# Optimization experiments

Hardware: AMD Instinct MI355X
Metric: run time of the kernel (lower is better)

## Reference

```python
import math
import jax, jax.numpy as jnp
import numpy as np

B, DIM, C, N = 1024, 512, 1000, 8
R = 0.05
WEIGHT_LAMBDA = 0.3
CN = C * N
TOPK = math.ceil(R * CN)  # 400


def setup_inputs() -> dict:
    key = jax.random.key(0)
    k1, k2, k3 = jax.random.split(key, 3)
    x = jax.random.normal(k1, (B, DIM), dtype=jnp.float32)
    # kaiming_uniform_(a=sqrt(5)) on a (DIM, CN) tensor: fan_in = CN (torch 2D fan_in = size(1)),
    # gain = sqrt(2/(1+a^2)) = sqrt(1/3), bound = gain * sqrt(3/fan_in)
    bound = math.sqrt(1.0 / 3.0) * math.sqrt(3.0 / CN)
    proxies = jax.random.uniform(k2, (DIM, CN), dtype=jnp.float32, minval=-bound, maxval=bound)
    target = jax.random.randint(k3, (B,), 0, C)
    return {"x": x, "proxies": proxies, "target": target}


def reference(x, proxies, target):
    instance_label = jnp.repeat(jnp.arange(C), N)  # (CN,)

    # F.normalize(Proxies, p=2, dim=0) with eps=1e-12 clamp
    norm = jnp.maximum(jnp.linalg.norm(proxies, axis=0, keepdims=True), 1e-12)
    centers = proxies / norm  # (DIM, CN)

    similarity = x @ centers  # (B, CN)

    positive_mask = (target[:, None] == instance_label[None, :]).astype(similarity.dtype)

    # topk over similarity boosted so all positives are included, then scatter 1s
    _, idx = jax.lax.top_k(similarity + 1000.0 * positive_mask, TOPK)  # (B, TOPK)
    mask = jnp.zeros_like(similarity).at[jnp.arange(B)[:, None], idx].set(1.0)
    mask = jax.lax.stop_gradient(mask)

    prob_a = mask * similarity  # (B, CN)
    # matmul with block one-hot y_instance_onehot == sum over the N proxies of each class
    logits = prob_a.reshape(B, C, N).sum(axis=-1)  # (B, C)

    logits_mask = jax.lax.stop_gradient((logits != 0.0).astype(logits.dtype))
    exp_l = jnp.exp(logits) * logits_mask
    predict = exp_l / (1e-8 + exp_l.sum(axis=1, keepdims=True))

    # sum(-y_onehot * log(predict+1e-20), 1) == -log(predict[b, target[b]] + 1e-20)
    loss_classify = jnp.mean(-jnp.log(predict[jnp.arange(B), target] + 1e-20))

    # regularizer: (centers.T @ centers) @ y_instance_onehot, fused as
    # centers.T @ (per-class sum of centers) -- identical math, avoids the CNxCN matrix
    centers_cls = centers.reshape(DIM, C, N).sum(axis=-1)  # (DIM, C)
    centers_logits = centers.T @ centers_cls  # (CN, C)
    logp = jax.nn.log_softmax(centers_logits, axis=1)
    reg = -jnp.mean(logp[jnp.arange(CN), instance_label])

    total = loss_classify + WEIGHT_LAMBDA * reg
    return (total, loss_classify)
```

## Files before the change

### kernel.cpp

```cpp
#include <hip/hip_runtime.h>
#include <hip/hip_bf16.h>
#include <math.h>

#define PB   1024
#define PDIM 512
#define PC   1000
#define PN   8
#define PCN  8000
#define PTOPK 400
#define NONPOS_K 392
#define NBIN 1024
#define CANDMAX 1024

typedef __bf16 bf16x8 __attribute__((ext_vector_type(8)));
typedef __bf16 bf16x4 __attribute__((ext_vector_type(4)));
typedef float  f32x4  __attribute__((ext_vector_type(4)));

__device__ static inline void async_load16(const __bf16* g, __bf16* l) {
    __builtin_amdgcn_global_load_lds(
        (const __attribute__((address_space(1))) void*)g,
        (__attribute__((address_space(3))) void*)l,
        16, 0, 0);
}

__global__ __launch_bounds__(256) void k_pre(const float* __restrict__ x,
                                             const float* __restrict__ P,
                                             __bf16* __restrict__ xb,
                                             float* __restrict__ ssqp,
                                             float* __restrict__ esd,
                                             float* __restrict__ padf,
                                             float* __restrict__ acc) {
    int b = blockIdx.x, tid = threadIdx.x;
    if (b == 0 && tid < 8) acc[tid] = 0.f;
    if (b < 512) {
        int i = b * 256 + tid;
        float4 v = ((const float4*)x)[i];
        bf16x4 o;
        o[0] = (__bf16)v.x; o[1] = (__bf16)v.y; o[2] = (__bf16)v.z; o[3] = (__bf16)v.w;
        ((bf16x4*)xb)[i] = o;
    } else if (b < 768) {
        int idx = b - 512;
        int slice = idx & 7, jb = idx >> 3;
        int j = jb * 256 + tid;
        if (j < PCN) {
            const float* p = P + (size_t)(slice * 64) * PCN + j;
            float ss = 0.f;
#pragma unroll 8
            for (int r = 0; r < 64; ++r) {
                float v = p[(size_t)r * PCN];
                ss = fmaf(v, v, ss);
            }
            ssqp[slice * PCN + j] = ss;
        }
    } else {
        int i = (b - 768) * 256 + tid;
        if (i < 16000) esd[i] = 0.f;
        else if (i < 16000 + 6144) padf[i - 16000] = 0.f;
    }
}

__global__ __launch_bounds__(256) void k_tpose(const float* __restrict__ P,
                                               const float* __restrict__ ssqp,
                                               __bf16* __restrict__ Pt,
                                               __bf16* __restrict__ ccls) {
    __shared__ float t[64][65];
    __shared__ float sinv[64];
    int tid = threadIdx.x;
    int tx = tid & 63, ty = tid >> 6;
    int j0 = blockIdx.x * 64, d0 = blockIdx.y * 64;
    if (tid < 64) {
        float sq = 0.f;
#pragma unroll
        for (int p2 = 0; p2 < 8; ++p2) sq += ssqp[p2 * PCN + j0 + tid];
        sinv[tid] = 1.0f / fmaxf(sqrtf(sq), 1e-12f);
    }
#pragma unroll
    for (int r = 0; r < 16; ++r) {
        int d = d0 + ty * 16 + r;
        t[ty * 16 + r][tx] = P[(size_t)d * PCN + j0 + tx];
    }
    __syncthreads();
    float cs0 = 0.f, cs1 = 0.f;
#pragma unroll
    for (int r = 0; r < 16; ++r) {
        int jl = ty * 16 + r;
        float val = t[tx][jl] * sinv[jl];
        Pt[(size_t)(j0 + jl) * PDIM + d0 + tx] = (__bf16)val;
        if (r < 8) cs0 += val; else cs1 += val;
    }
    int c0 = (j0 >> 3) + ty * 2;
    ccls[(size_t)c0 * PDIM + d0 + tx] = (__bf16)cs0;
    ccls[(size_t)(c0 + 1) * PDIM + d0 + tx] = (__bf16)cs1;
}

__global__ __launch_bounds__(256, 2) void k_gemms(const __bf16* __restrict__ xb,
                                                  const __bf16* __restrict__ Pt,
                                                  const __bf16* __restrict__ ccls,
                                                  __bf16* __restrict__ simb,
                                                  float* __restrict__ esum,
                                                  float* __restrict__ diag) {
    __shared__ __bf16 Xs[2][128 * 32];
    __shared__ __bf16 Ps[2][128 * 32];
    __shared__ __bf16 Cs[2][128 * 32];
    int tid = threadIdx.x;
    int w = tid >> 6, lane = tid & 63;
    int wr = w >> 1, wc = w & 1;
    int quad = lane >> 4, l15 = lane & 15;
    int id = blockIdx.x;
    int jt = id >> 3, t = id & 7;
    int m0 = t * 128;
    int n0 = jt * 128;

    f32x4 accS[4][4] = {};
    f32x4 accC[4][4] = {};

#define STAGE3(buf, k0) {                                                     \
    _Pragma("unroll")                                                         \
    for (int pass = 0; pass < 2; ++pass) {                                    \
        int cc_ = pass * 256 + w * 64 + lane;                                 \
        int row_ = cc_ >> 2, ko_ = (cc_ & 3) * 8;                             \
        async_load16(xb + (size_t)(m0 + row_) * PDIM + (k0) + ko_,            \
                     &Xs[buf][cc_ * 8]);                                      \
        int prow = n0 + row_; if (prow > PCN - 1) prow = PCN - 1;             \
        async_load16(Pt + (size_t)prow * PDIM + (k0) + ko_,                   \
                     &Ps[buf][cc_ * 8]);                                      \
        async_load16(ccls + (size_t)(m0 + row_) * PDIM + (k0) + ko_,          \
                     &Cs[buf][cc_ * 8]);                                      \
    } }

    STAGE3(0, 0)
    for (int it = 0; it < 16; ++it) {
        int cur = it & 1;
        __syncthreads();
        if (it < 15) STAGE3(cur ^ 1, (it + 1) * 32)
        bf16x8 xa[4], pb[4], pa[4], cb[4];
#pragma unroll
        for (int i = 0; i < 4; ++i) {
            xa[i] = *(const bf16x8*)&Xs[cur][(wr * 64 + i * 16 + l15) * 32 + quad * 8];
            pb[i] = *(const bf16x8*)&Ps[cur][(wc * 64 + i * 16 + l15) * 32 + quad * 8];
            pa[i] = *(const bf16x8*)&Ps[cur][(wr * 64 + i * 16 + l15) * 32 + quad * 8];
            cb[i] = *(const bf16x8*)&Cs[cur][(wc * 64 + i * 16 + l15) * 32 + quad * 8];
        }
#pragma unroll
        for (int i = 0; i < 4; ++i)
#pragma unroll
            for (int j = 0; j < 4; ++j) {
                accS[i][j] = __builtin_amdgcn_mfma_f32_16x16x32_bf16(
                    xa[i], pb[j], accS[i][j], 0, 0, 0);
                accC[i][j] = __builtin_amdgcn_mfma_f32_16x16x32_bf16(
                    pa[i], cb[j], accC[i][j], 0, 0, 0);
            }
    }
#undef STAGE3

#pragma unroll
    for (int i = 0; i < 4; ++i) {
        int r0 = m0 + wr * 64 + i * 16 + quad * 4;
#pragma unroll
        for (int j = 0; j < 4; ++j) {
            int cc = n0 + wc * 64 + j * 16 + l15;
            if (cc < PCN) {
#pragma unroll
                for (int r = 0; r < 4; ++r)
                    simb[(size_t)(r0 + r) * PCN + cc] = (__bf16)accS[i][j][r];
            }
        }
    }
#pragma unroll
    for (int i = 0; i < 4; ++i) {
        int r0 = n0 + wr * 64 + i * 16 + quad * 4;
        float psum[4] = {0.f, 0.f, 0.f, 0.f};
#pragma unroll
        for (int j = 0; j < 4; ++j) {
            int cc = m0 + wc * 64 + j * 16 + l15;
            bool cvalid = (cc < PC);
#pragma unroll
            for (int r = 0; r < 4; ++r) {
                float v = accC[i][j][r];
                psum[r] += cvalid ? expf(v) : 0.f;
                int rr = r0 + r;
                if (cvalid && rr < PCN && cc == (rr >> 3)) diag[rr] = v;
            }
        }
#pragma unroll
        for (int off = 1; off < 16; off <<= 1)
#pragma unroll
            for (int r = 0; r < 4; ++r)
                psum[r] += __shfl_xor(psum[r], off, 64);
        if (l15 == 0) {
#pragma unroll
            for (int r = 0; r < 4; ++r) {
                int rr = r0 + r;
                if (rr < PCN) atomicAdd(&esum[rr], psum[r]);
            }
        }
    }
}

__global__ __launch_bounds__(256) void k_rowloss(const __bf16* __restrict__ sim,
                                                 const int* __restrict__ target,
                                                 float* __restrict__ acc) {
    __shared__ unsigned hist[NBIN];
    __shared__ float redf[8];
    __shared__ unsigned wtot[4];
    __shared__ float cand[CANDMAX];
    __shared__ unsigned candn;
    __shared__ int s_bin, s_A;
    __shared__ float s_tau;
    __shared__ int s_gt, s_eq;
    __shared__ float s_et;

    int b = blockIdx.x, tid = threadIdx.x;
    int lane = tid & 63, wv = tid >> 6;
    const bf16x8* row8 = (const bf16x8*)(sim + (size_t)b * PCN);
    int targ = target[b];

#pragma unroll
    for (int k = 0; k < 4; ++k) hist[tid + 256 * k] = 0u;
    if (tid == 0) candn = 0u;

    float pv[4][8];
    float lmn = INFINITY, lmx = -INFINITY;
#pragma unroll
    for (int k = 0; k < 4; ++k) {
        int c = tid + 256 * k;
        if (c < PC) {
            bf16x8 vv = row8[c];
#pragma unroll
            for (int n = 0; n < 8; ++n) pv[k][n] = (float)vv[n];
            if (c != targ) {
#pragma unroll
                for (int n = 0; n < 8; ++n) {
                    lmn = fminf(lmn, pv[k][n]);
                    lmx = fmaxf(lmx, pv[k][n]);
                }
            }
        } else {
#pragma unroll
            for (int n = 0; n < 8; ++n) pv[k][n] = 0.f;
        }
    }
    for (int off = 32; off; off >>= 1) {
        lmn = fminf(lmn, __shfl_down(lmn, off, 64));
        lmx = fmaxf(lmx, __shfl_down(lmx, off, 64));
    }
    if (lane == 0) { redf[wv] = lmn; redf[4 + wv] = lmx; }
    __syncthreads();
    float lo = fminf(fminf(redf[0], redf[1]), fminf(redf[2], redf[3]));
    float hi = fmaxf(fmaxf(redf[4], redf[5]), fmaxf(redf[6], redf[7]));
    float range = hi - lo;
    float scale = (range > 0.f) ? (float)NBIN / range : 0.f;

#pragma unroll
    for (int k = 0; k < 4; ++k) {
        int c = tid + 256 * k;
        if (c < PC && c != targ) {
#pragma unroll
            for (int n = 0; n < 8; ++n) {
                int bin = (int)((pv[k][n] - lo) * scale);
                bin = bin < 0 ? 0 : (bin > NBIN - 1 ? NBIN - 1 : bin);
                atomicAdd(&hist[bin], 1u);
            }
        }
    }
    __syncthreads();

    int b0 = tid * 4;
    unsigned h0 = hist[b0], h1 = hist[b0 + 1], h2 = hist[b0 + 2], h3 = hist[b0 + 3];
    unsigned l3 = h3, l2 = h2 + l3, l1 = h1 + l2, l0 = h0 + l1;
    unsigned T = l0;
#pragma unroll
    for (int step = 1; step < 64; step <<= 1) {
        unsigned u = __shfl_down(T, step, 64);
        if (lane + step < 64) T += u;
    }
    if (lane == 0) wtot[wv] = T;
    __syncthreads();
    unsigned tail = 0;
#pragma unroll
    for (int w2 = 0; w2 < 4; ++w2) if (w2 > wv) tail += wtot[w2];
    unsigned E = T - l0 + tail;
    {
        unsigned sfx[4] = {l0 + E, l1 + E, l2 + E, l3 + E};
        unsigned nxt[4] = {l1 + E, l2 + E, l3 + E, E};
#pragma unroll
        for (int i = 0; i < 4; ++i)
            if (sfx[i] >= NONPOS_K && nxt[i] < NONPOS_K) {
                s_bin = b0 + i;
                s_A = (int)nxt[i];
            }
    }
    __syncthreads();
    int tbin = s_bin, A = s_A;

#pragma unroll
    for (int k = 0; k < 4; ++k) {
        int c = tid + 256 * k;
        if (c < PC && c != targ) {
#pragma unroll
            for (int n = 0; n < 8; ++n) {
                int bin = (int)((pv[k][n] - lo) * scale);
                bin = bin < 0 ? 0 : (bin > NBIN - 1 ? NBIN - 1 : bin);
                if (bin == tbin) {
                    unsigned idx = atomicAdd(&candn, 1u);
                    if (idx < CANDMAX) cand[idx] = pv[k][n];
                }
            }
        }
    }
    __syncthreads();
    int m = (int)candn; if (m > CANDMAX) m = CANDMAX;
    int rank = NONPOS_K - A;
    for (int ci = tid; ci < m; ci += 256) {
        float val = cand[ci];
        int g = 0, e = 0;
        for (int i = 0; i < m; ++i) {
            g += cand[i] > val;
            e += cand[i] == val;
        }
        if (g < rank && rank <= g + e) { s_tau = val; s_gt = g; s_eq = e; }
    }
    __syncthreads();
    float tau = s_tau;
    int cgt = A + s_gt, ceq = s_eq;
    int rem = NONPOS_K - cgt;
    bool all_eq = (rem >= ceq);

    int offs[4] = {0, 0, 0, 0};
    if (!all_eq) {
        unsigned chunk_base = 0;
#pragma unroll
        for (int k = 0; k < 4; ++k) {
            int c = tid + 256 * k;
            unsigned tn = 0;
            if (c < PC && c != targ) {
#pragma unroll
                for (int n = 0; n < 8; ++n) tn += (pv[k][n] == tau) ? 1u : 0u;
            }
            unsigned inc = tn;
#pragma unroll
            for (int step = 1; step < 64; step <<= 1) {
                unsigned u = __shfl_up(inc, step, 64);
                if (lane >= step) inc += u;
            }
            __syncthreads();
            if (lane == 63) wtot[wv] = inc;
            __syncthreads();
            unsigned base = 0;
#pragma unroll
            for (int w2 = 0; w2 < 4; ++w2) if (w2 < wv) base += wtot[w2];
            offs[k] = (int)(chunk_base + base + inc - tn);
            chunk_base += wtot[0] + wtot[1] + wtot[2] + wtot[3];
        }
    }

    float psum = 0.f;
#pragma unroll
    for (int k = 0; k < 4; ++k) {
        int c = tid + 256 * k;
        if (c >= PC) continue;
        float lg = 0.f;
        if (c == targ) {
#pragma unroll
            for (int n = 0; n < 8; ++n) lg += pv[k][n];
        } else {
#pragma unroll
            for (int n = 0; n < 8; ++n) {
                float v = pv[k][n];
                bool sel = v > tau;
                if (!sel && v == tau) {
                    if (all_eq) sel = true;
                    else { sel = (offs[k] < rem); offs[k]++; }
                }
                if (sel) lg += v;
            }
        }
        float e = (lg != 0.0f) ? expf(lg) : 0.0f;
        psum += e;
        if (c == targ) s_et = e;
    }
    for (int off = 32; off; off >>= 1) psum += __shfl_down(psum, off, 64);
    if (lane == 0) redf[wv] = psum;
    __syncthreads();
    if (tid == 0) {
        float denom = 1e-8f + redf[0] + redf[1] + redf[2] + redf[3];
        atomicAdd(acc, -logf(s_et / denom + 1e-20f));
    }
}

__global__ __launch_bounds__(256) void k_final(const float* __restrict__ esum,
                                               const float* __restrict__ diag,
                                               const float* __restrict__ acc,
                                               float* __restrict__ out) {
    __shared__ float redf[4];
    int tid = threadIdx.x, lane = tid & 63, wv = tid >> 6;
    float s = 0.f;
    for (int j = tid; j < PCN; j += 256)
        s += logf(esum[j]) - diag[j];
    for (int off = 32; off; off >>= 1) s += __shfl_down(s, off, 64);
    if (lane == 0) redf[wv] = s;
    __syncthreads();
    if (tid == 0) {
        float rg = (redf[0] + redf[1] + redf[2] + redf[3]) * (1.0f / PCN);
        float lc = acc[0] * (1.0f / PB);
        out[0] = lc + 0.3f * rg;
        out[1] = lc;
    }
}

extern "C" void kernel_launch(void* const* d_in, const int* in_sizes, int n_in,
                              void* d_out, int out_size, void* d_ws, size_t ws_size,
                              hipStream_t stream) {
    const float* x       = (const float*)d_in[0];
    const float* proxies = (const float*)d_in[1];
    const int*   target  = (const int*)d_in[2];
    float* out = (float*)d_out;
    float* ws  = (float*)d_ws;

    float*  acc   = ws;
    float*  ssqp  = ws + 64;
    float*  esum  = ws + 64064;
    float*  diag  = ws + 72064;
    __bf16* xb    = (__bf16*)(ws + 80064);
    __bf16* cclsb = (__bf16*)(ws + 342208);
    __bf16* Pt    = (__bf16*)(ws + 604352);
    __bf16* simb  = (__bf16*)(ws + 2652352);

    float* padf = (float*)cclsb + 256000;

    k_pre<<<856, 256, 0, stream>>>(x, proxies, xb, ssqp, esum, padf, acc);
    k_tpose<<<dim3(125, 8), 256, 0, stream>>>(proxies, ssqp, Pt, cclsb);

    k_gemms<<<504, 256, 0, stream>>>(xb, Pt, cclsb, simb, esum, diag);

    k_rowloss<<<PB, 256, 0, stream>>>(simb, target, acc);
    k_final<<<1, 256, 0, stream>>>(esum, diag, acc, out);
}
```

Baseline: 139.8 us.

## Split fused dual GEMM into independent 256x256 tiled GEMM blocks with swizzled LDS

Replaces the kernel that computed the similarity and regularizer GEMMs together in 128x128 tiles with one launch where each block computes a single 256x256 tile of one of the two GEMMs. Blocks 0-127 do x@centers and blocks 128-255 do centers.T@centers_cls. It uses 512 threads, a K-step of 64, XOR-swizzled LDS to avoid bank conflicts, explicit waitcnt/barrier double buffering, and raised MFMA priority. The aim is more reuse per loaded byte, less LDS traffic and better MFMA utilization. The cost is that only 256 blocks run at 2 per CU, so occupancy is uneven, and the larger accumulator footprint raises register pressure.

```diff
diff --git a/kernel.cpp b/kernel.cpp
--- a/kernel.cpp
+++ b/kernel.cpp
@@ -93,105 +93,132 @@
     ccls[(size_t)(c0 + 1) * PDIM + d0 + tx] = (__bf16)cs1;
 }
 
-__global__ __launch_bounds__(256, 2) void k_gemms(const __bf16* __restrict__ xb,
-                                                  const __bf16* __restrict__ Pt,
-                                                  const __bf16* __restrict__ ccls,
-                                                  __bf16* __restrict__ simb,
-                                                  float* __restrict__ esum,
-                                                  float* __restrict__ diag) {
-    __shared__ __bf16 Xs[2][128 * 32];
-    __shared__ __bf16 Ps[2][128 * 32];
-    __shared__ __bf16 Cs[2][128 * 32];
+__global__ __launch_bounds__(512, 2) void k_gemms2(const __bf16* __restrict__ xb,
+                                                   const __bf16* __restrict__ Pt,
+                                                   const __bf16* __restrict__ ccls,
+                                                   __bf16* __restrict__ simb,
+                                                   float* __restrict__ esum,
+                                                   float* __restrict__ diag) {
+    __shared__ __align__(16) __bf16 As[2][256 * 64];
+    __shared__ __align__(16) __bf16 Bs[2][256 * 64];
+
     int tid = threadIdx.x;
     int w = tid >> 6, lane = tid & 63;
-    int wr = w >> 1, wc = w & 1;
+    int wr = w >> 2, wc = w & 3;
     int quad = lane >> 4, l15 = lane & 15;
-    int id = blockIdx.x;
-    int jt = id >> 3, t = id & 7;
-    int m0 = t * 128;
-    int n0 = jt * 128;
-
-    f32x4 accS[4][4] = {};
-    f32x4 accC[4][4] = {};
-
-#define STAGE3(buf, k0) {                                                     \
-    _Pragma("unroll")                                                         \
-    for (int pass = 0; pass < 2; ++pass) {                                    \
-        int cc_ = pass * 256 + w * 64 + lane;                                 \
-        int row_ = cc_ >> 2, ko_ = (cc_ & 3) * 8;                             \
-        async_load16(xb + (size_t)(m0 + row_) * PDIM + (k0) + ko_,            \
-                     &Xs[buf][cc_ * 8]);                                      \
-        int prow = n0 + row_; if (prow > PCN - 1) prow = PCN - 1;             \
-        async_load16(Pt + (size_t)prow * PDIM + (k0) + ko_,                   \
-                     &Ps[buf][cc_ * 8]);                                      \
-        async_load16(ccls + (size_t)(m0 + row_) * PDIM + (k0) + ko_,          \
-                     &Cs[buf][cc_ * 8]);                                      \
+
+    int bid = blockIdx.x;
+    bool is_sim = bid < 128;
+    int M0, N0, Amax, Bmax;
+    const __bf16 *Ab, *Bb;
+    if (is_sim) {
+        int mt = bid >> 5, nt = bid & 31;
+        M0 = mt * 256; N0 = nt * 256;
+        Ab = xb; Bb = Pt; Amax = PB - 1; Bmax = PCN - 1;
+    } else {
+        int b2 = bid - 128;
+        int mt = b2 >> 2, nt = b2 & 3;
+        M0 = mt * 256; N0 = nt * 256;
+        Ab = Pt; Bb = ccls; Amax = PCN - 1; Bmax = 1023;
+    }
+
+    f32x4 acc[8][4] = {};
+
+#define STAGE(kt_) {                                                         \
+    int k0_ = (kt_) * 64, bb_ = (kt_) & 1;                                   \
+    _Pragma("unroll")                                                        \
+    for (int p_ = 0; p_ < 4; ++p_) {                                         \
+        int idx_ = p_ * 512 + tid;                                           \
+        int row_ = idx_ >> 3, sp_ = idx_ & 7;                                \
+        int gk_ = ((sp_ ^ (row_ & 7)) << 3) + k0_;                           \
+        int ga_ = M0 + row_; if (ga_ > Amax) ga_ = Amax;                     \
+        async_load16(Ab + (size_t)ga_ * PDIM + gk_, &As[bb_][idx_ * 8]);     \
+        int gb_ = N0 + row_; if (gb_ > Bmax) gb_ = Bmax;                     \
+        async_load16(Bb + (size_t)gb_ * PDIM + gk_, &Bs[bb_][idx_ * 8]);     \
     } }
 
-    STAGE3(0, 0)
-    for (int it = 0; it < 16; ++it) {
-        int cur = it & 1;
-        __syncthreads();
-        if (it < 15) STAGE3(cur ^ 1, (it + 1) * 32)
-        bf16x8 xa[4], pb[4], pa[4], cb[4];
-#pragma unroll
-        for (int i = 0; i < 4; ++i) {
-            xa[i] = *(const bf16x8*)&Xs[cur][(wr * 64 + i * 16 + l15) * 32 + quad * 8];
-            pb[i] = *(const bf16x8*)&Ps[cur][(wc * 64 + i * 16 + l15) * 32 + quad * 8];
-            pa[i] = *(const bf16x8*)&Ps[cur][(wr * 64 + i * 16 + l15) * 32 + quad * 8];
-            cb[i] = *(const bf16x8*)&Cs[cur][(wc * 64 + i * 16 + l15) * 32 + quad * 8];
-        }
-#pragma unroll
-        for (int i = 0; i < 4; ++i)
-#pragma unroll
-            for (int j = 0; j < 4; ++j) {
-                accS[i][j] = __builtin_amdgcn_mfma_f32_16x16x32_bf16(
-                    xa[i], pb[j], accS[i][j], 0, 0, 0);
-                accC[i][j] = __builtin_amdgcn_mfma_f32_16x16x32_bf16(
-                    pa[i], cb[j], accC[i][j], 0, 0, 0);
-            }
-    }
-#undef STAGE3
-
-#pragma unroll
-    for (int i = 0; i < 4; ++i) {
-        int r0 = m0 + wr * 64 + i * 16 + quad * 4;
-#pragma unroll
-        for (int j = 0; j < 4; ++j) {
-            int cc = n0 + wc * 64 + j * 16 + l15;
-            if (cc < PCN) {
+    STAGE(0)
+    for (int kt = 0; kt < 8; ++kt) {
+        int cur = kt & 1;
+        asm volatile("s_waitcnt lgkmcnt(0)" ::: "memory");
+        __builtin_amdgcn_s_barrier();
+        if (kt < 7) {
+            STAGE(kt + 1)
+            asm volatile("s_waitcnt vmcnt(8)" ::: "memory");
+        } else {
+            asm volatile("s_waitcnt vmcnt(0)" ::: "memory");
+        }
+        __builtin_amdgcn_s_barrier();
+
+#pragma unroll
+        for (int ks = 0; ks < 2; ++ks) {
+            bf16x8 af[8], bfr[4];
+#pragma unroll
+            for (int mi = 0; mi < 8; ++mi) {
+                int row = wr * 128 + mi * 16 + l15;
+                af[mi] = *(const bf16x8*)&As[cur][(row << 6) +
+                         ((((ks << 2) + quad) ^ (row & 7)) << 3)];
+            }
+#pragma unroll
+            for (int nj = 0; nj < 4; ++nj) {
+                int row = wc * 64 + nj * 16 + l15;
+                bfr[nj] = *(const bf16x8*)&Bs[cur][(row << 6) +
+                          ((((ks << 2) + quad) ^ (row & 7)) << 3)];
+            }
+            __builtin_amdgcn_s_setprio(1);
+#pragma unroll
+            for (int mi = 0; mi < 8; ++mi)
+#pragma unroll
+                for (int nj = 0; nj < 4; ++nj)
+                    acc[mi][nj] = __builtin_amdgcn_mfma_f32_16x16x32_bf16(
+                        af[mi], bfr[nj], acc[mi][nj], 0, 0, 0);
+            __builtin_amdgcn_s_setprio(0);
+        }
+    }
+#undef STAGE
+
+    if (is_sim) {
+#pragma unroll
+        for (int mi = 0; mi < 8; ++mi) {
+            int r0 = M0 + wr * 128 + mi * 16 + quad * 4;
+#pragma unroll
+            for (int nj = 0; nj < 4; ++nj) {
+                int cc = N0 + wc * 64 + nj * 16 + l15;
+                if (cc < PCN) {
+#pragma unroll
+                    for (int r = 0; r < 4; ++r)
+                        simb[(size_t)(r0 + r) * PCN + cc] = (__bf16)acc[mi][nj][r];
+                }
+            }
+        }
+    } else {
+#pragma unroll
+        for (int mi = 0; mi < 8; ++mi) {
+            int r0 = M0 + wr * 128 + mi * 16 + quad * 4;
+            float psum[4] = {0.f, 0.f, 0.f, 0.f};
+#pragma unroll
+            for (int nj = 0; nj < 4; ++nj) {
+                int cc = N0 + wc * 64 + nj * 16 + l15;
+                bool cvalid = (cc < PC);
+#pragma unroll
+                for (int r = 0; r < 4; ++r) {
+                    float v = acc[mi][nj][r];
+                    psum[r] += cvalid ? expf(v) : 0.f;
+                    int rr = r0 + r;
+                    if (cvalid && rr < PCN && cc == (rr >> 3)) diag[rr] = v;
+                }
+            }
+#pragma unroll
+            for (int off = 1; off < 16; off <<= 1)
 #pragma unroll
                 for (int r = 0; r < 4; ++r)
-                    simb[(size_t)(r0 + r) * PCN + cc] = (__bf16)accS[i][j][r];
-            }
-        }
-    }
-#pragma unroll
-    for (int i = 0; i < 4; ++i) {
-        int r0 = n0 + wr * 64 + i * 16 + quad * 4;
-        float psum[4] = {0.f, 0.f, 0.f, 0.f};
-#pragma unroll
-        for (int j = 0; j < 4; ++j) {
-            int cc = m0 + wc * 64 + j * 16 + l15;
-            bool cvalid = (cc < PC);
-#pragma unroll
-            for (int r = 0; r < 4; ++r) {
-                float v = accC[i][j][r];
-                psum[r] += cvalid ? expf(v) : 0.f;
-                int rr = r0 + r;
-                if (cvalid && rr < PCN && cc == (rr >> 3)) diag[rr] = v;
-            }
-        }
-#pragma unroll
-        for (int off = 1; off < 16; off <<= 1)
-#pragma unroll
-            for (int r = 0; r < 4; ++r)
-                psum[r] += __shfl_xor(psum[r], off, 64);
-        if (l15 == 0) {
-#pragma unroll
-            for (int r = 0; r < 4; ++r) {
-                int rr = r0 + r;
-                if (rr < PCN) atomicAdd(&esum[rr], psum[r]);
+                    psum[r] += __shfl_xor(psum[r], off, 64);
+            if (l15 == 0) {
+#pragma unroll
+                for (int r = 0; r < 4; ++r) {
+                    int rr = r0 + r;
+                    if (rr < PCN) atomicAdd(&esum[rr], psum[r]);
+                }
             }
         }
     }
@@ -431,7 +458,7 @@
     k_pre<<<856, 256, 0, stream>>>(x, proxies, xb, ssqp, esum, padf, acc);
     k_tpose<<<dim3(125, 8), 256, 0, stream>>>(proxies, ssqp, Pt, cclsb);
 
-    k_gemms<<<504, 256, 0, stream>>>(xb, Pt, cclsb, simb, esum, diag);
+    k_gemms2<<<256, 512, 0, stream>>>(xb, Pt, cclsb, simb, esum, diag);
 
     k_rowloss<<<PB, 256, 0, stream>>>(simb, target, acc);
     k_final<<<1, 256, 0, stream>>>(esum, diag, acc, out);
```

Result: no change. 138.6 us (-0.9%).
